# Performance work log

Hardware: AMD Instinct MI355X
Metric: run time of the kernel (lower is better)

The kernel has to match this reference:

```python
import jax, jax.numpy as jnp
import numpy as np

D_MODEL = 1024
EXPAND = 2
D_INNER = EXPAND * D_MODEL  # 2048
HEADDIM = 64
NHEADS = D_INNER // HEADDIM  # 32
D_STATE = 64
D_CONV = 4
BATCH = 2
SEQ_LEN = 1024
LN_EPS = 1e-5


def setup_inputs() -> dict:
    key = jax.random.key(0)
    ks = jax.random.split(key, 12)
    s = 0.02
    return {
        "hidden_states": jax.random.normal(ks[0], (BATCH, SEQ_LEN, D_MODEL), jnp.float32),
        "in_proj_w": jax.random.normal(ks[1], (2 * D_INNER, D_MODEL), jnp.float32) * s,
        "conv_w": jax.random.normal(ks[2], (D_INNER, 1, D_CONV), jnp.float32) * 0.1,
        "conv_b": jax.random.normal(ks[3], (D_INNER,), jnp.float32) * 0.01,
        "A_log": jnp.zeros((NHEADS,), jnp.float32),  # log(ones) as in init
        "dt_w": jax.random.normal(ks[4], (NHEADS, D_INNER), jnp.float32) * s,
        "dt_b": jax.random.normal(ks[5], (NHEADS,), jnp.float32) * 0.1,
        "B_w": jax.random.normal(ks[6], (NHEADS * D_STATE, D_INNER), jnp.float32) * s,
        "C_w": jax.random.normal(ks[7], (NHEADS * D_STATE, D_INNER), jnp.float32) * s,
        "D": jnp.ones((NHEADS,), jnp.float32),
        "ln_w": jnp.ones((D_INNER,), jnp.float32),
        "ln_b": jnp.zeros((D_INNER,), jnp.float32),
        "out_proj_w": jax.random.normal(ks[8], (D_MODEL, D_INNER), jnp.float32) * s,
    }


def _layernorm(x, w, b):
    mu = jnp.mean(x, axis=-1, keepdims=True)
    var = jnp.var(x, axis=-1, keepdims=True)
    return (x - mu) * jax.lax.rsqrt(var + LN_EPS) * w + b


def _forward(hidden_states, in_proj_w, conv_w, conv_b, A_log, dt_w, dt_b,
             B_w, C_w, D, ln_w, ln_b, out_proj_w):
    B_, L, _ = hidden_states.shape
    xz = hidden_states @ in_proj_w.T                       # [B, L, 2*d_inner]
    x, z = jnp.split(xz, 2, axis=-1)

    # depthwise causal conv1d (torch pads both sides, slices [:L] == causal left-pad)
    x_ncl = jnp.transpose(x, (0, 2, 1))                    # [B, d_inner, L]
    x_conv = jax.lax.conv_general_dilated(
        x_ncl, conv_w, window_strides=(1,), padding=[(D_CONV - 1, 0)],
        dimension_numbers=("NCH", "OIH", "NCH"), feature_group_count=D_INNER)
    x_conv = x_conv + conv_b[None, :, None]
    x = jnp.transpose(x_conv, (0, 2, 1))                   # [B, L, d_inner]
    x = jax.nn.silu(x)

    dt = jax.nn.softplus(x @ dt_w.T + dt_b)                # [B, L, H]
    Bm = (x @ B_w.T).reshape(B_, L, NHEADS, D_STATE)       # [B, L, H, N]
    Cm = (x @ C_w.T).reshape(B_, L, NHEADS, D_STATE)       # [B, L, H, N]
    xh = x.reshape(B_, L, NHEADS, HEADDIM)                 # [B, L, H, P]
    A = -jnp.exp(A_log)                                    # [H]

    h0 = jnp.zeros((B_, NHEADS, HEADDIM, D_STATE), x.dtype)

    def step(h, inp):
        x_t, dt_t, B_t, C_t = inp  # [B,H,P], [B,H], [B,H,N], [B,H,N]
        A_bar = jnp.exp(A[None, :] * dt_t)[..., None, None]           # [B,H,1,1]
        h = A_bar * h + (dt_t[..., None, None] * B_t[:, :, None, :]) * x_t[..., None]
        y_t = jnp.einsum("bhpn,bhn->bhp", h, C_t) + D[None, :, None] * x_t
        return h, y_t

    xs = (jnp.transpose(xh, (1, 0, 2, 3)), jnp.transpose(dt, (1, 0, 2)),
          jnp.transpose(Bm, (1, 0, 2, 3)), jnp.transpose(Cm, (1, 0, 2, 3)))
    h_final, y = jax.lax.scan(step, h0, xs)                # y: [L, B, H, P]
    y = jnp.transpose(y, (1, 0, 2, 3)).reshape(B_, L, D_INNER)

    y = _layernorm(y, ln_w, ln_b)
    y = y * jax.nn.silu(z)
    output = y @ out_proj_w.T
    return output, h_final


def reference(hidden_states, in_proj_w, conv_w, conv_b, A_log, dt_w, dt_b,
              B_w, C_w, D, ln_w, ln_b, out_proj_w):
    return _forward(hidden_states, in_proj_w, conv_w, conv_b, A_log, dt_w, dt_b,
                    B_w, C_w, D, ln_w, ln_b, out_proj_w)
```

## Files before the change

### kernel.cpp

```cpp
#include <hip/hip_runtime.h>
#include <math.h>

#define BATCH 2
#define SEQLEN 1024
#define DMODEL 1024
#define DINNER 2048
#define NHEADS 32
#define HEADDIM 64
#define DSTATE 64
#define NTOK (BATCH * SEQLEN)
#define OUT_ELEMS (BATCH * SEQLEN * DMODEL)
#define NCHUNK 16
#define LDP 72

typedef unsigned short bf16u;
typedef __attribute__((ext_vector_type(8))) short short8;
typedef __attribute__((ext_vector_type(4))) float f32x4;

__device__ __forceinline__ float b2f(short u) {
  return __uint_as_float(((unsigned)(unsigned short)u) << 16);
}
__device__ __forceinline__ unsigned short f2b(float f) {
  unsigned u = __float_as_uint(f);
  u += 0x7fff + ((u >> 16) & 1);
  return (unsigned short)(u >> 16);
}

__device__ __forceinline__ void gload16(const void* g, void* l) {
  __builtin_amdgcn_global_load_lds(
      (const __attribute__((address_space(1))) unsigned int*)g,
      (__attribute__((address_space(3))) unsigned int*)l, 16, 0, 0);
}

__device__ __forceinline__ void stv(float* p, float v) { *p = v; }
__device__ __forceinline__ void stv(bf16u* p, float v) { *p = f2b(v); }

__global__ __launch_bounds__(256) void cvt_bf16(const float* __restrict__ in,
                                                bf16u* __restrict__ out, int n) {
  const int i = (blockIdx.x * 256 + threadIdx.x) * 8;
  if (i >= n) return;
  const float4 a = *(const float4*)(in + i);
  const float4 b = *(const float4*)(in + i + 4);
  short8 o;
  o[0] = f2b(a.x); o[1] = f2b(a.y); o[2] = f2b(a.z); o[3] = f2b(a.w);
  o[4] = f2b(b.x); o[5] = f2b(b.y); o[6] = f2b(b.z); o[7] = f2b(b.w);
  *(short8*)(out + i) = o;
}

template <typename OutT>
__global__ __launch_bounds__(256) void gemm_mfma(
    const bf16u* __restrict__ A, const bf16u* __restrict__ B,
    OutT* __restrict__ C, int M, int N, int Ksub, int lda, int ldb,
    size_t zstrideC) {
  __shared__ bf16u sA[3][128 * 32];
  __shared__ bf16u sB[3][64 * 32];
  const int t = threadIdx.x;
  const int lane = t & 63, wave = t >> 6;
  const int bm = blockIdx.y * 128, bn = blockIdx.x * 64;
  const int wr = wave >> 1, wc = wave & 1;
  const int kbase = blockIdx.z * Ksub;
  OutT* Cz = C + (size_t)blockIdx.z * zstrideC;

  const int ra0 = bm + (t >> 2), ra1 = bm + 64 + (t >> 2);
  int rb0 = bn + (t >> 2);
  rb0 = rb0 < N ? rb0 : N - 1;
  const int kc = (((t & 3) ^ ((t >> 4) & 3))) * 8;

  const bf16u* Ap0 = A + (size_t)ra0 * lda + kbase + kc;
  const bf16u* Ap1 = A + (size_t)ra1 * lda + kbase + kc;
  const bf16u* Bp0 = B + (size_t)rb0 * ldb + kbase + kc;
  const int ldsoff = (wave * 64) * 8;

#define STAGE(buf, k0)                                   \
  do {                                                   \
    gload16(Ap0 + (k0), sA[buf] + ldsoff);               \
    gload16(Ap1 + (k0), sA[buf] + 2048 + ldsoff);        \
    gload16(Bp0 + (k0), sB[buf] + ldsoff);               \
  } while (0)

  const f32x4 zero = {0.f, 0.f, 0.f, 0.f};
  f32x4 acc[4][2];
#pragma unroll
  for (int m = 0; m < 4; ++m)
#pragma unroll
    for (int n = 0; n < 2; ++n) acc[m][n] = zero;

  const int ln15 = lane & 15, kq = lane >> 4;
  const int kswz = ((kq ^ ((ln15 >> 2) & 3))) * 8;
  const int nt = Ksub >> 5;

  STAGE(0, 0);
  STAGE(1, 32);
  int curb = 0;
  for (int it = 0; it < nt; ++it) {
    if (it + 2 < nt) {
      const int nb = (it + 2) % 3;
      STAGE(nb, (it + 2) * 32);
      asm volatile("s_waitcnt vmcnt(6)" ::: "memory");
    } else if (it + 1 < nt) {
      asm volatile("s_waitcnt vmcnt(3)" ::: "memory");
    } else {
      asm volatile("s_waitcnt vmcnt(0)" ::: "memory");
    }
    __builtin_amdgcn_s_barrier();
    const bf16u* pA = sA[curb];
    const bf16u* pB = sB[curb];
    short8 af[4], bfr[2];
#pragma unroll
    for (int m = 0; m < 4; ++m)
      af[m] = *(const short8*)&pA[(wr * 64 + m * 16 + ln15) * 32 + kswz];
#pragma unroll
    for (int n = 0; n < 2; ++n)
      bfr[n] = *(const short8*)&pB[(wc * 32 + n * 16 + ln15) * 32 + kswz];
    __builtin_amdgcn_s_setprio(1);
#pragma unroll
    for (int m = 0; m < 4; ++m)
#pragma unroll
      for (int n = 0; n < 2; ++n)
        acc[m][n] = __builtin_amdgcn_mfma_f32_16x16x32_bf16(af[m], bfr[n], acc[m][n], 0, 0, 0);
    __builtin_amdgcn_s_setprio(0);
    asm volatile("s_waitcnt lgkmcnt(0)" ::: "memory");
    __builtin_amdgcn_s_barrier();
    curb = (curb == 2) ? 0 : curb + 1;
  }
#undef STAGE

  const int rbase = bm + wr * 64, cbase = bn + wc * 32;
#pragma unroll
  for (int m = 0; m < 4; ++m) {
#pragma unroll
    for (int n = 0; n < 2; ++n) {
      const int col = cbase + n * 16 + ln15;
      if (col < N) {
#pragma unroll
        for (int r = 0; r < 4; ++r) {
          const int row = rbase + m * 16 + kq * 4 + r;
          stv(&Cz[(size_t)row * N + col], acc[m][n][r]);
        }
      }
    }
  }
}

__global__ __launch_bounds__(256) void add4_f32(
    const float* __restrict__ a, const float* __restrict__ b,
    const float* __restrict__ c, const float* __restrict__ d,
    float* __restrict__ o, int n) {
  const int i = (blockIdx.x * 256 + threadIdx.x) * 4;
  if (i >= n) return;
  const float4 x = *(const float4*)(a + i);
  const float4 y = *(const float4*)(b + i);
  const float4 z = *(const float4*)(c + i);
  const float4 w = *(const float4*)(d + i);
  *(float4*)(o + i) = make_float4(x.x + y.x + z.x + w.x, x.y + y.y + z.y + w.y,
                                  x.z + y.z + z.z + w.z, x.w + y.w + z.w + w.w);
}

__global__ __launch_bounds__(256) void conv_silu(
    const bf16u* __restrict__ xzb, const float* __restrict__ cw,
    const float* __restrict__ cb, bf16u* __restrict__ xcb) {
  const int i = blockIdx.x * 256 + threadIdx.x;
  const int c8 = (i & 255) * 8;
  const int tok = i >> 8;
  const int l = tok & (SEQLEN - 1);
  const bf16u* xp = xzb + (size_t)tok * (2 * DINNER) + c8;
  const short8 zer = {0, 0, 0, 0, 0, 0, 0, 0};
  const short8 x0 = *(const short8*)xp;
  const short8 x1 = (l >= 1) ? *(const short8*)(xp - 1 * (2 * DINNER)) : zer;
  const short8 x2 = (l >= 2) ? *(const short8*)(xp - 2 * (2 * DINNER)) : zer;
  const short8 x3 = (l >= 3) ? *(const short8*)(xp - 3 * (2 * DINNER)) : zer;
  short8 ob;
#pragma unroll
  for (int j = 0; j < 8; ++j) {
    const float4 w = *(const float4*)(cw + (c8 + j) * 4);
    float acc = cb[c8 + j] + w.w * b2f(x0[j]);
    acc += w.z * b2f(x1[j]);
    acc += w.y * b2f(x2[j]);
    acc += w.x * b2f(x3[j]);
    const float s = acc / (1.f + __expf(-acc));
    ob[j] = (short)f2b(s);
  }
  *(short8*)(xcb + (size_t)tok * DINNER + c8) = ob;
}

__global__ __launch_bounds__(256) void dt_act(float* __restrict__ dtb,
                                              const float* __restrict__ dt_b) {
  const int i = blockIdx.x * 256 + threadIdx.x;
  if (i >= NTOK * NHEADS) return;
  const float v = dtb[i] + dtb[i + 65536] + dtb[i + 131072] + dtb[i + 196608] +
                  dt_b[i & (NHEADS - 1)];
  dtb[i] = (v > 20.f) ? v : log1pf(expf(v));
}

__global__ __launch_bounds__(256) void chunk_intra(
    const bf16u* __restrict__ xcb, const bf16u* __restrict__ BCb,
    const float* __restrict__ dtb, const float* __restrict__ A_log,
    bf16u* __restrict__ ybb, float* __restrict__ Sbuf,
    float* __restrict__ rbuf, float* __restrict__ lambuf) {
  __shared__ bf16u sC[64 * LDP], sB[64 * LDP], sXT[64 * LDP];
  __shared__ bf16u sWBT[64 * LDP], sP[64 * LDP];
  __shared__ float sS[64], sDt[64], sW[64];

  const int blk = blockIdx.x;
  const int bh = blk >> 4, c = blk & (NCHUNK - 1);
  const int b = bh >> 5, h = bh & (NHEADS - 1);
  const int t = threadIdx.x, lane = t & 63, wave = t >> 6;
  const int t0 = b * SEQLEN + c * 64;
  const size_t rowbase = (size_t)t0 * DINNER + h * 64;
  const size_t rowBC = (size_t)t0 * 4096 + h * 64;

  if (wave == 0) {
    const float dtv = dtb[(size_t)(t0 + lane) * NHEADS + h];
    const float Ah = -__expf(A_log[h]);
    float s = Ah * dtv;
#pragma unroll
    for (int off = 1; off < 64; off <<= 1) {
      const float o = __shfl_up(s, off);
      if (lane >= off) s += o;
    }
    const float stot = __shfl(s, 63);
    sS[lane] = s;
    sDt[lane] = dtv;
    sW[lane] = __expf(stot - s) * dtv;
    rbuf[(size_t)blk * 64 + lane] = __expf(s);
    if (lane == 0) lambuf[blk] = __expf(stot);
  } else if (wave == 1) {
#pragma unroll
    for (int it = 0; it < 8; ++it) {
      const int slot = it * 64 + lane;
      const int r = slot >> 3, c8 = (slot & 7) * 8;
      *(short8*)&sC[r * LDP + c8] =
          *(const short8*)&BCb[rowBC + 2048 + (size_t)r * 4096 + c8];
    }
  } else if (wave == 2) {
#pragma unroll
    for (int it = 0; it < 8; ++it) {
      const int slot = it * 64 + lane;
      const int r = slot >> 3, c8 = (slot & 7) * 8;
      *(short8*)&sB[r * LDP + c8] =
          *(const short8*)&BCb[rowBC + (size_t)r * 4096 + c8];
    }
  } else {
#pragma unroll
    for (int it = 0; it < 8; ++it) {
      const int slot = it * 64 + lane;
      const int j = slot >> 3, p0 = (slot & 7) * 8;
      const short8 v = *(const short8*)&xcb[rowbase + (size_t)j * DINNER + p0];
#pragma unroll
      for (int k = 0; k < 8; ++k) sXT[(p0 + k) * LDP + j] = v[k];
    }
  }
  __syncthreads();

  {
    const int j = t >> 2, n0 = (t & 3) * 16;
    const float wj = sW[j];
#pragma unroll
    for (int k = 0; k < 16; ++k)
      sWBT[(n0 + k) * LDP + j] = f2b(wj * b2f(sB[j * LDP + n0 + k]));
  }
  const int ln15 = lane & 15, kq = lane >> 4;
  const int i0 = wave * 16;
  const f32x4 zero = {0.f, 0.f, 0.f, 0.f};
  {
    f32x4 g[4];
#pragma unroll
    for (int jf = 0; jf < 4; ++jf) g[jf] = zero;
#pragma unroll
    for (int k0 = 0; k0 < 64; k0 += 32) {
      const short8 a = *(const short8*)&sC[(i0 + ln15) * LDP + k0 + kq * 8];
#pragma unroll
      for (int jf = 0; jf < 4; ++jf) {
        const short8 bb = *(const short8*)&sB[(jf * 16 + ln15) * LDP + k0 + kq * 8];
        g[jf] = __builtin_amdgcn_mfma_f32_16x16x32_bf16(a, bb, g[jf], 0, 0, 0);
      }
    }
#pragma unroll
    for (int jf = 0; jf < 4; ++jf) {
      const int j = jf * 16 + ln15;
      const float sj = sS[j], dtj = sDt[j];
#pragma unroll
      for (int r = 0; r < 4; ++r) {
        const int i = i0 + kq * 4 + r;
        const float v = (j <= i) ? g[jf][r] * __expf(sS[i] - sj) * dtj : 0.f;
        sP[i * LDP + j] = f2b(v);
      }
    }
  }
  __syncthreads();

  f32x4 yi[4], ss[4];
#pragma unroll
  for (int f = 0; f < 4; ++f) { yi[f] = zero; ss[f] = zero; }
#pragma unroll
  for (int k0 = 0; k0 < 64; k0 += 32) {
    const short8 ap = *(const short8*)&sP[(i0 + ln15) * LDP + k0 + kq * 8];
    const short8 ax = *(const short8*)&sXT[(i0 + ln15) * LDP + k0 + kq * 8];
#pragma unroll
    for (int f = 0; f < 4; ++f) {
      const short8 bx = *(const short8*)&sXT[(f * 16 + ln15) * LDP + k0 + kq * 8];
      const short8 bw = *(const short8*)&sWBT[(f * 16 + ln15) * LDP + k0 + kq * 8];
      yi[f] = __builtin_amdgcn_mfma_f32_16x16x32_bf16(ap, bx, yi[f], 0, 0, 0);
      ss[f] = __builtin_amdgcn_mfma_f32_16x16x32_bf16(ax, bw, ss[f], 0, 0, 0);
    }
  }
  bf16u* yb = ybb + (size_t)blk * 4096;
  float* sb = Sbuf + (size_t)blk * 4096;
#pragma unroll
  for (int f = 0; f < 4; ++f) {
#pragma unroll
    for (int r = 0; r < 4; ++r) {
      const int row = i0 + kq * 4 + r;
      const int col = f * 16 + ln15;
      yb[row * 64 + col] = f2b(yi[f][r]);
      sb[row * 64 + col] = ss[f][r];
    }
  }
}

__global__ __launch_bounds__(256) void chunk_scan(
    const float* __restrict__ Sbuf, const float* __restrict__ lambuf,
    bf16u* __restrict__ Hprevb, float* __restrict__ hf) {
  const int bh = blockIdx.x;
  const int t = threadIdx.x;
  const int e0 = t * 16;
  float H[16];
#pragma unroll
  for (int j = 0; j < 16; ++j) H[j] = 0.f;

  float4 cur[4];
  float lam;
  {
    const float4* sp = (const float4*)(Sbuf + (size_t)(bh * NCHUNK) * 4096 + e0);
#pragma unroll
    for (int q = 0; q < 4; ++q) cur[q] = sp[q];
    lam = lambuf[bh * NCHUNK];
  }
  for (int c = 0; c < NCHUNK; ++c) {
    float4 nxt[4];
    float lamn = 0.f;
    if (c < NCHUNK - 1) {
      const float4* sp = (const float4*)(Sbuf + (size_t)(bh * NCHUNK + c + 1) * 4096 + e0);
#pragma unroll
      for (int q = 0; q < 4; ++q) nxt[q] = sp[q];
      lamn = lambuf[bh * NCHUNK + c + 1];
    }
    short8 o0, o1;
#pragma unroll
    for (int j = 0; j < 8; ++j) o0[j] = (short)f2b(H[j]);
#pragma unroll
    for (int j = 0; j < 8; ++j) o1[j] = (short)f2b(H[8 + j]);
    *(short8*)&Hprevb[(size_t)(bh * NCHUNK + c) * 4096 + e0] = o0;
    *(short8*)&Hprevb[(size_t)(bh * NCHUNK + c) * 4096 + e0 + 8] = o1;
#pragma unroll
    for (int q = 0; q < 4; ++q) {
      H[q * 4 + 0] = lam * H[q * 4 + 0] + cur[q].x;
      H[q * 4 + 1] = lam * H[q * 4 + 1] + cur[q].y;
      H[q * 4 + 2] = lam * H[q * 4 + 2] + cur[q].z;
      H[q * 4 + 3] = lam * H[q * 4 + 3] + cur[q].w;
    }
#pragma unroll
    for (int q = 0; q < 4; ++q) cur[q] = nxt[q];
    lam = lamn;
  }
  float* hp = hf + (size_t)bh * 4096 + e0;
#pragma unroll
  for (int q = 0; q < 4; ++q)
    *(float4*)(hp + q * 4) =
        make_float4(H[q * 4], H[q * 4 + 1], H[q * 4 + 2], H[q * 4 + 3]);
}

__global__ __launch_bounds__(256) void chunk_inter(
    const bf16u* __restrict__ BCb, const bf16u* __restrict__ Hprevb,
    const bf16u* __restrict__ xcb, const bf16u* __restrict__ ybb,
    const float* __restrict__ rbuf, const float* __restrict__ Dvec,
    bf16u* __restrict__ yout) {
  __shared__ bf16u sC[64 * LDP], sH[64 * LDP];
  __shared__ float sR[64];
  const int blk = blockIdx.x;
  const int bh = blk >> 4, c = blk & (NCHUNK - 1);
  const int b = bh >> 5, h = bh & (NHEADS - 1);
  const int t = threadIdx.x, lane = t & 63, wave = t >> 6;
  const int t0 = b * SEQLEN + c * 64;
  const size_t rowbase = (size_t)t0 * DINNER + h * 64;
  const size_t rowBC = (size_t)t0 * 4096 + h * 64;

#pragma unroll
  for (int it = 0; it < 2; ++it) {
    const int slot = it * 256 + t;
    const int r = slot >> 3, c8 = (slot & 7) * 8;
    *(short8*)&sC[r * LDP + c8] =
        *(const short8*)&BCb[rowBC + 2048 + (size_t)r * 4096 + c8];
    *(short8*)&sH[r * LDP + c8] =
        *(const short8*)&Hprevb[(size_t)blk * 4096 + slot * 8];
  }
  if (t < 64) sR[t] = rbuf[(size_t)blk * 64 + t];
  __syncthreads();

  const int ln15 = lane & 15, kq = lane >> 4;
  const int i0 = wave * 16;
  const f32x4 zero = {0.f, 0.f, 0.f, 0.f};
  f32x4 acc[4];
#pragma unroll
  for (int f = 0; f < 4; ++f) acc[f] = zero;
#pragma unroll
  for (int k0 = 0; k0 < 64; k0 += 32) {
    const short8 a = *(const short8*)&sC[(i0 + ln15) * LDP + k0 + kq * 8];
#pragma unroll
    for (int f = 0; f < 4; ++f) {
      const short8 bh8 = *(const short8*)&sH[(f * 16 + ln15) * LDP + k0 + kq * 8];
      acc[f] = __builtin_amdgcn_mfma_f32_16x16x32_bf16(a, bh8, acc[f], 0, 0, 0);
    }
  }
  const float Dh = Dvec[h];
  const bf16u* yb = ybb + (size_t)blk * 4096;
#pragma unroll
  for (int f = 0; f < 4; ++f) {
    const int p = f * 16 + ln15;
#pragma unroll
    for (int r = 0; r < 4; ++r) {
      const int i = i0 + kq * 4 + r;
      const float xv = b2f((short)xcb[rowbase + (size_t)i * DINNER + p]);
      const float y = b2f((short)yb[i * 64 + p]) + sR[i] * acc[f][r] + Dh * xv;
      yout[rowbase + (size_t)i * DINNER + p] = f2b(y);
    }
  }
}

__global__ __launch_bounds__(256) void ln_gate(
    const bf16u* __restrict__ y, const bf16u* __restrict__ xzb,
    const float* __restrict__ lnw, const float* __restrict__ lnb,
    bf16u* __restrict__ out) {
  const int tok = blockIdx.x;
  const int t = threadIdx.x;
  const short8 yv8 = *(const short8*)(y + (size_t)tok * DINNER + t * 8);
  const short8 zv8 = *(const short8*)(xzb + (size_t)tok * (2 * DINNER) + DINNER + t * 8);
  float v[8];
  float s = 0.f, s2 = 0.f;
#pragma unroll
  for (int j = 0; j < 8; ++j) {
    v[j] = b2f(yv8[j]);
    s += v[j];
    s2 += v[j] * v[j];
  }
#pragma unroll
  for (int off = 32; off > 0; off >>= 1) {
    s += __shfl_down(s, off);
    s2 += __shfl_down(s2, off);
  }
  __shared__ float ws[4], ws2[4];
  const int wid = t >> 6;
  if ((t & 63) == 0) { ws[wid] = s; ws2[wid] = s2; }
  __syncthreads();
  const float mean = (ws[0] + ws[1] + ws[2] + ws[3]) * (1.f / DINNER);
  const float m2 = (ws2[0] + ws2[1] + ws2[2] + ws2[3]) * (1.f / DINNER);
  const float rstd = rsqrtf(m2 - mean * mean + 1e-5f);
  const float4 w0 = *(const float4*)(lnw + t * 8);
  const float4 w1 = *(const float4*)(lnw + t * 8 + 4);
  const float4 b0 = *(const float4*)(lnb + t * 8);
  const float4 b1 = *(const float4*)(lnb + t * 8 + 4);
  const float wv[8] = {w0.x, w0.y, w0.z, w0.w, w1.x, w1.y, w1.z, w1.w};
  const float bv[8] = {b0.x, b0.y, b0.z, b0.w, b1.x, b1.y, b1.z, b1.w};
  short8 o;
#pragma unroll
  for (int j = 0; j < 8; ++j) {
    const float zn = b2f(zv8[j]);
    const float gate = zn / (1.f + __expf(-zn));
    o[j] = (short)f2b(((v[j] - mean) * rstd * wv[j] + bv[j]) * gate);
  }
  *(short8*)(out + (size_t)tok * DINNER + t * 8) = o;
}

extern "C" void kernel_launch(void* const* d_in, const int* in_sizes, int n_in,
                              void* d_out, int out_size, void* d_ws, size_t ws_size,
                              hipStream_t stream) {
  const float* hidden = (const float*)d_in[0];
  const float* in_proj_w = (const float*)d_in[1];
  const float* conv_w = (const float*)d_in[2];
  const float* conv_b = (const float*)d_in[3];
  const float* A_log = (const float*)d_in[4];
  const float* dt_w = (const float*)d_in[5];
  const float* dt_b = (const float*)d_in[6];
  const float* B_w = (const float*)d_in[7];
  const float* C_w = (const float*)d_in[8];
  const float* Dv = (const float*)d_in[9];
  const float* ln_w = (const float*)d_in[10];
  const float* ln_b = (const float*)d_in[11];
  const float* out_proj_w = (const float*)d_in[12];

  float* out = (float*)d_out;
  float* f = (float*)d_ws;
  const size_t M1 = 1u << 20;

  bf16u* xzb    = (bf16u*)(f + 0);
  bf16u* xcb    = (bf16u*)(f + 4 * M1);
  bf16u* BCb    = (bf16u*)(f + 6 * M1);
  bf16u* wBCb   = (bf16u*)(f + 10 * M1);
  bf16u* ybb    = (bf16u*)(f + 10 * M1);
  float* outp   = f + 6 * M1;
  bf16u* wInb   = (bf16u*)(f + 14 * M1);
  bf16u* hiddenb= (bf16u*)(f + 16 * M1);
  bf16u* wdtb   = (bf16u*)(f + 17 * M1);
  float* Sbuf   = f + 14 * M1;
  bf16u* ygb    = (bf16u*)(f + 14 * M1);
  bf16u* yscb   = (bf16u*)(f + 16 * M1);
  bf16u* Hprevb = (bf16u*)(f + 18 * M1);
  bf16u* wOb    = (bf16u*)(f + 20 * M1);
  float* dtbuf  = f + 21 * M1;
  float* rbuf   = f + 21 * M1 + 262144;
  float* lambuf = f + 21 * M1 + 327680;

  float* hf = out + OUT_ELEMS;

  cvt_bf16<<<1024, 256, 0, stream>>>(hidden, hiddenb, 2 * M1);
  cvt_bf16<<<2048, 256, 0, stream>>>(in_proj_w, wInb, 4 * M1);
  cvt_bf16<<<2048, 256, 0, stream>>>(B_w, wBCb, 4 * M1);
  cvt_bf16<<<2048, 256, 0, stream>>>(C_w, wBCb + 4 * M1, 4 * M1);
  cvt_bf16<<<1024, 256, 0, stream>>>(out_proj_w, wOb, 2 * M1);
  cvt_bf16<<<32, 256, 0, stream>>>(dt_w, wdtb, NHEADS * DINNER);

  gemm_mfma<bf16u><<<dim3(64, 16, 1), 256, 0, stream>>>(
      hiddenb, wInb, xzb, NTOK, 2 * DINNER, DMODEL, DMODEL, DMODEL, 0);
  conv_silu<<<2048, 256, 0, stream>>>(xzb, conv_w, conv_b, xcb);
  gemm_mfma<float><<<dim3(1, 16, 4), 256, 0, stream>>>(
      xcb, wdtb, dtbuf, NTOK, NHEADS, DINNER / 4, DINNER, DINNER,
      (size_t)NTOK * NHEADS);
  gemm_mfma<bf16u><<<dim3(64, 16, 1), 256, 0, stream>>>(
      xcb, wBCb, BCb, NTOK, 2 * DINNER, DINNER, DINNER, DINNER, 0);
  dt_act<<<(NTOK * NHEADS) / 256, 256, 0, stream>>>(dtbuf, dt_b);
  chunk_intra<<<BATCH * NHEADS * NCHUNK, 256, 0, stream>>>(
      xcb, BCb, dtbuf, A_log, ybb, Sbuf, rbuf, lambuf);
  chunk_scan<<<BATCH * NHEADS, 256, 0, stream>>>(Sbuf, lambuf, Hprevb, hf);
  chunk_inter<<<BATCH * NHEADS * NCHUNK, 256, 0, stream>>>(
      BCb, Hprevb, xcb, ybb, rbuf, Dv, yscb);
  ln_gate<<<NTOK, 256, 0, stream>>>(yscb, xzb, ln_w, ln_b, ygb);
  gemm_mfma<float><<<dim3(16, 16, 4), 256, 0, stream>>>(
      ygb, wOb, outp, NTOK, DMODEL, DINNER / 4, DINNER, DINNER,
      (size_t)2 * M1);
  add4_f32<<<2048, 256, 0, stream>>>(outp, outp + 2 * M1, outp + 4 * M1,
                                     outp + 6 * M1, out, OUT_ELEMS);
}
```

Before: 211.3 us.

## Double GEMM K-tile, merge weight conversions, halve out-proj split-K

The GEMM kernel now stages 64-wide K tiles instead of 32-wide, so it does half as many barrier and wait iterations, at the cost of twice the shared memory per stage. The six separate fp32-to-bf16 conversion launches become one launch that picks its source by index range, which removes launch overhead. The out_proj GEMM uses split-K of 2 instead of 4, so the reduction reads two partial buffers instead of four. In exchange the out_proj GEMM runs fewer blocks, and the larger LDS footprint may lower occupancy.

```diff
diff --git a/kernel.cpp b/kernel.cpp
--- a/kernel.cpp
+++ b/kernel.cpp
@@ -35,16 +35,29 @@
 __device__ __forceinline__ void stv(float* p, float v) { *p = v; }
 __device__ __forceinline__ void stv(bf16u* p, float v) { *p = f2b(v); }
 
-__global__ __launch_bounds__(256) void cvt_bf16(const float* __restrict__ in,
-                                                bf16u* __restrict__ out, int n) {
-  const int i = (blockIdx.x * 256 + threadIdx.x) * 8;
-  if (i >= n) return;
-  const float4 a = *(const float4*)(in + i);
-  const float4 b = *(const float4*)(in + i + 4);
+__global__ __launch_bounds__(256) void cvt_all(
+    const float* __restrict__ s0, bf16u* __restrict__ d0,
+    const float* __restrict__ s1, bf16u* __restrict__ d1,
+    const float* __restrict__ s2, bf16u* __restrict__ d2,
+    const float* __restrict__ s3, bf16u* __restrict__ d3,
+    const float* __restrict__ s4, bf16u* __restrict__ d4,
+    const float* __restrict__ s5, bf16u* __restrict__ d5) {
+  const size_t M1 = 1u << 20;
+  size_t i = (size_t)(blockIdx.x * 256 + threadIdx.x) * 8;
+  const float* src; bf16u* dst; size_t off;
+  if (i < 2 * M1)       { src = s0; dst = d0; off = i; }
+  else if (i < 6 * M1)  { src = s1; dst = d1; off = i - 2 * M1; }
+  else if (i < 10 * M1) { src = s2; dst = d2; off = i - 6 * M1; }
+  else if (i < 14 * M1) { src = s3; dst = d3; off = i - 10 * M1; }
+  else if (i < 16 * M1) { src = s4; dst = d4; off = i - 14 * M1; }
+  else if (i < 16 * M1 + 65536) { src = s5; dst = d5; off = i - 16 * M1; }
+  else return;
+  const float4 a = *(const float4*)(src + off);
+  const float4 b = *(const float4*)(src + off + 4);
   short8 o;
   o[0] = f2b(a.x); o[1] = f2b(a.y); o[2] = f2b(a.z); o[3] = f2b(a.w);
   o[4] = f2b(b.x); o[5] = f2b(b.y); o[6] = f2b(b.z); o[7] = f2b(b.w);
-  *(short8*)(out + i) = o;
+  *(short8*)(dst + off) = o;
 }
 
 template <typename OutT>
@@ -52,8 +65,8 @@
     const bf16u* __restrict__ A, const bf16u* __restrict__ B,
     OutT* __restrict__ C, int M, int N, int Ksub, int lda, int ldb,
     size_t zstrideC) {
-  __shared__ bf16u sA[3][128 * 32];
-  __shared__ bf16u sB[3][64 * 32];
+  __shared__ bf16u sA[3][128 * 64];
+  __shared__ bf16u sB[3][64 * 64];
   const int t = threadIdx.x;
   const int lane = t & 63, wave = t >> 6;
   const int bm = blockIdx.y * 128, bn = blockIdx.x * 64;
@@ -71,11 +84,14 @@
   const bf16u* Bp0 = B + (size_t)rb0 * ldb + kbase + kc;
   const int ldsoff = (wave * 64) * 8;
 
-#define STAGE(buf, k0)                                   \
-  do {                                                   \
-    gload16(Ap0 + (k0), sA[buf] + ldsoff);               \
-    gload16(Ap1 + (k0), sA[buf] + 2048 + ldsoff);        \
-    gload16(Bp0 + (k0), sB[buf] + ldsoff);               \
+#define STAGE(buf, k0)                                        \
+  do {                                                        \
+    gload16(Ap0 + (k0), sA[buf] + ldsoff);                    \
+    gload16(Ap1 + (k0), sA[buf] + 2048 + ldsoff);             \
+    gload16(Ap0 + (k0) + 32, sA[buf] + 4096 + ldsoff);        \
+    gload16(Ap1 + (k0) + 32, sA[buf] + 6144 + ldsoff);        \
+    gload16(Bp0 + (k0), sB[buf] + ldsoff);                    \
+    gload16(Bp0 + (k0) + 32, sB[buf] + 2048 + ldsoff);        \
   } while (0)
 
   const f32x4 zero = {0.f, 0.f, 0.f, 0.f};
@@ -87,38 +103,41 @@
 
   const int ln15 = lane & 15, kq = lane >> 4;
   const int kswz = ((kq ^ ((ln15 >> 2) & 3))) * 8;
-  const int nt = Ksub >> 5;
+  const int nt = Ksub >> 6;
 
   STAGE(0, 0);
-  STAGE(1, 32);
+  STAGE(1, 64);
   int curb = 0;
   for (int it = 0; it < nt; ++it) {
     if (it + 2 < nt) {
       const int nb = (it + 2) % 3;
-      STAGE(nb, (it + 2) * 32);
+      STAGE(nb, (it + 2) * 64);
+      asm volatile("s_waitcnt vmcnt(12)" ::: "memory");
+    } else if (it + 1 < nt) {
       asm volatile("s_waitcnt vmcnt(6)" ::: "memory");
-    } else if (it + 1 < nt) {
-      asm volatile("s_waitcnt vmcnt(3)" ::: "memory");
     } else {
       asm volatile("s_waitcnt vmcnt(0)" ::: "memory");
     }
     __builtin_amdgcn_s_barrier();
     const bf16u* pA = sA[curb];
     const bf16u* pB = sB[curb];
-    short8 af[4], bfr[2];
-#pragma unroll
-    for (int m = 0; m < 4; ++m)
-      af[m] = *(const short8*)&pA[(wr * 64 + m * 16 + ln15) * 32 + kswz];
-#pragma unroll
-    for (int n = 0; n < 2; ++n)
-      bfr[n] = *(const short8*)&pB[(wc * 32 + n * 16 + ln15) * 32 + kswz];
-    __builtin_amdgcn_s_setprio(1);
-#pragma unroll
-    for (int m = 0; m < 4; ++m)
+#pragma unroll
+    for (int p = 0; p < 2; ++p) {
+      short8 af[4], bfr[2];
+#pragma unroll
+      for (int m = 0; m < 4; ++m)
+        af[m] = *(const short8*)&pA[p * 4096 + (wr * 64 + m * 16 + ln15) * 32 + kswz];
 #pragma unroll
       for (int n = 0; n < 2; ++n)
-        acc[m][n] = __builtin_amdgcn_mfma_f32_16x16x32_bf16(af[m], bfr[n], acc[m][n], 0, 0, 0);
-    __builtin_amdgcn_s_setprio(0);
+        bfr[n] = *(const short8*)&pB[p * 2048 + (wc * 32 + n * 16 + ln15) * 32 + kswz];
+      __builtin_amdgcn_s_setprio(1);
+#pragma unroll
+      for (int m = 0; m < 4; ++m)
+#pragma unroll
+        for (int n = 0; n < 2; ++n)
+          acc[m][n] = __builtin_amdgcn_mfma_f32_16x16x32_bf16(af[m], bfr[n], acc[m][n], 0, 0, 0);
+      __builtin_amdgcn_s_setprio(0);
+    }
     asm volatile("s_waitcnt lgkmcnt(0)" ::: "memory");
     __builtin_amdgcn_s_barrier();
     curb = (curb == 2) ? 0 : curb + 1;
@@ -142,18 +161,14 @@
   }
 }
 
-__global__ __launch_bounds__(256) void add4_f32(
-    const float* __restrict__ a, const float* __restrict__ b,
-    const float* __restrict__ c, const float* __restrict__ d,
-    float* __restrict__ o, int n) {
+__global__ __launch_bounds__(256) void add_f32(const float* __restrict__ a,
+                                               const float* __restrict__ b,
+                                               float* __restrict__ o, int n) {
   const int i = (blockIdx.x * 256 + threadIdx.x) * 4;
   if (i >= n) return;
   const float4 x = *(const float4*)(a + i);
   const float4 y = *(const float4*)(b + i);
-  const float4 z = *(const float4*)(c + i);
-  const float4 w = *(const float4*)(d + i);
-  *(float4*)(o + i) = make_float4(x.x + y.x + z.x + w.x, x.y + y.y + z.y + w.y,
-                                  x.z + y.z + z.z + w.z, x.w + y.w + z.w + w.w);
+  *(float4*)(o + i) = make_float4(x.x + y.x, x.y + y.y, x.z + y.z, x.w + y.w);
 }
 
 __global__ __launch_bounds__(256) void conv_silu(
@@ -512,12 +527,9 @@
 
   float* hf = out + OUT_ELEMS;
 
-  cvt_bf16<<<1024, 256, 0, stream>>>(hidden, hiddenb, 2 * M1);
-  cvt_bf16<<<2048, 256, 0, stream>>>(in_proj_w, wInb, 4 * M1);
-  cvt_bf16<<<2048, 256, 0, stream>>>(B_w, wBCb, 4 * M1);
-  cvt_bf16<<<2048, 256, 0, stream>>>(C_w, wBCb + 4 * M1, 4 * M1);
-  cvt_bf16<<<1024, 256, 0, stream>>>(out_proj_w, wOb, 2 * M1);
-  cvt_bf16<<<32, 256, 0, stream>>>(dt_w, wdtb, NHEADS * DINNER);
+  cvt_all<<<8224, 256, 0, stream>>>(hidden, hiddenb, in_proj_w, wInb,
+                                    B_w, wBCb, C_w, wBCb + 4 * M1,
+                                    out_proj_w, wOb, dt_w, wdtb);
 
   gemm_mfma<bf16u><<<dim3(64, 16, 1), 256, 0, stream>>>(
       hiddenb, wInb, xzb, NTOK, 2 * DINNER, DMODEL, DMODEL, DMODEL, 0);
@@ -534,9 +546,8 @@
   chunk_inter<<<BATCH * NHEADS * NCHUNK, 256, 0, stream>>>(
       BCb, Hprevb, xcb, ybb, rbuf, Dv, yscb);
   ln_gate<<<NTOK, 256, 0, stream>>>(yscb, xzb, ln_w, ln_b, ygb);
-  gemm_mfma<float><<<dim3(16, 16, 4), 256, 0, stream>>>(
-      ygb, wOb, outp, NTOK, DMODEL, DINNER / 4, DINNER, DINNER,
+  gemm_mfma<float><<<dim3(16, 16, 2), 256, 0, stream>>>(
+      ygb, wOb, outp, NTOK, DMODEL, DINNER / 2, DINNER, DINNER,
       (size_t)2 * M1);
-  add4_f32<<<2048, 256, 0, stream>>>(outp, outp + 2 * M1, outp + 4 * M1,
-                                     outp + 6 * M1, out, OUT_ELEMS);
-}
+  add_f32<<<2048, 256, 0, stream>>>(outp, outp + 2 * M1, out, OUT_ELEMS);
+}
```

Measured after the change: 200.2 us. 5.2% less time.
